# Kernel optimization log

Measured on AMD Instinct MI355X. Metric: run time of the kernel, lower is better.

Reference implementation:

```python
import jax, jax.numpy as jnp
import numpy as np
import math

B, N, E, D = 8, 2048, 2048, 128
MAX_K = 8
HYPER_DIM = 128
LN_EPS = 1e-5


def _sinusoidal_pe(max_pos, dim):
    pe = np.zeros((max_pos, dim), dtype=np.float32)
    position = np.arange(max_pos, dtype=np.float32)[:, None]
    div_term = np.exp(np.arange(0, dim, 2, dtype=np.float32) * (-math.log(10000.0) / dim))
    pe[:, 0::2] = np.sin(position * div_term)
    pe[:, 1::2] = np.cos(position * div_term)
    return jnp.asarray(pe)


def setup_inputs() -> dict:
    key = jax.random.key(0)
    ks = jax.random.split(key, 24)
    s = 0.05
    inp = {
        'x_v': jax.random.normal(ks[0], (B, N, D), jnp.float32),
        'x_e': jax.random.normal(ks[1], (B, E, D), jnp.float32),
        'incidence': (jax.random.uniform(ks[2], (B, N, E), jnp.float32) < 0.01).astype(jnp.float32),
        'suffix_normalizer': jax.random.uniform(ks[3], (B, N), jnp.float32) * 20.0,
        'edge_orders': 1 + jax.random.randint(ks[4], (B, E), 0, MAX_K),
        'node_mask': jax.random.randint(ks[5], (B, N), 0, 2) > 0,
        'edge_mask': jax.random.randint(ks[6], (B, E), 0, 2) > 0,
        'pe1_table': _sinusoidal_pe(MAX_K + 1, D),
        'pe2_table': _sinusoidal_pe(2, D),
        'bias_b': jax.random.uniform(ks[7], (1, D), jnp.float32, -1, 1) / math.sqrt(D),
    }
    i = 8
    for m in ('mlp1', 'mlp2', 'mlp3'):
        inp[m + '_W1'] = jax.random.normal(ks[i], (D, HYPER_DIM), jnp.float32) * s; i += 1
        inp[m + '_b1'] = jnp.zeros((HYPER_DIM,), jnp.float32)
        inp[m + '_W2'] = jax.random.normal(ks[i], (HYPER_DIM, D), jnp.float32) * s; i += 1
        inp[m + '_b2'] = jnp.zeros((D,), jnp.float32)
    for n in ('norm1', 'norm2', 'norm3'):
        inp[n + '_g'] = jnp.ones((D,), jnp.float32)
        inp[n + '_b'] = jnp.zeros((D,), jnp.float32)
    return inp


def _ln(x, g, b):
    mu = jnp.mean(x, axis=-1, keepdims=True)
    var = jnp.mean(jnp.square(x - mu), axis=-1, keepdims=True)
    return (x - mu) * jax.lax.rsqrt(var + LN_EPS) * g + b


def _mlp(x, W1, b1, W2, b2):
    return jax.nn.relu(x @ W1 + b1) @ W2 + b2


def reference(x_v, x_e, incidence, suffix_normalizer, edge_orders, node_mask, edge_mask,
              pe1_table, pe2_table, bias_b,
              mlp1_W1, mlp1_b1, mlp1_W2, mlp1_b2,
              mlp2_W1, mlp2_b1, mlp2_W2, mlp2_b2,
              mlp3_W1, mlp3_b1, mlp3_W2, mlp3_b2,
              norm1_g, norm1_b, norm2_g, norm2_b, norm3_g, norm3_b):
    nm = node_mask[..., None]  # [B,N,1]
    em = edge_mask[..., None]  # [B,E,1]
    x_v = jnp.where(nm, x_v, 0.0)
    x_e = jnp.where(em, x_e, 0.0)
    pe1_k1 = pe1_table[1][None, None, :]          # [1,1,D]
    pe1_k = pe1_table[edge_orders]                # [B,E,D]
    x_v = x_v + _mlp(_ln(x_v, norm1_g, norm1_b) + pe1_k1, mlp1_W1, mlp1_b1, mlp1_W2, mlp1_b2)
    x_e = x_e + _mlp(_ln(x_e, norm1_g, norm1_b) + pe1_k, mlp1_W1, mlp1_b1, mlp1_W2, mlp1_b2)
    x_v = jnp.where(nm, x_v, 0.0)
    x_e = jnp.where(em, x_e, 0.0)
    agg = jnp.einsum('bne,bed->bnd', incidence, x_e)
    x1 = x_v + agg / (1.0 + suffix_normalizer[..., None])
    pe2_s1 = pe2_table[1][None, None, :]
    x1 = x1 + _mlp(_ln(x1, norm2_g, norm2_b) + pe2_s1, mlp2_W1, mlp2_b1, mlp2_W2, mlp2_b2)
    x = jnp.where(nm, x1, 0.0)
    x = x + _mlp(_ln(x, norm3_g, norm3_b), mlp3_W1, mlp3_b1, mlp3_W2, mlp3_b2)
    x = x + bias_b
    x = jnp.where(nm, x, 0.0)
    return x
```

## Files before the change

### kernel.cpp

```cpp
#include <hip/hip_runtime.h>
#include <stdint.h>

#define BB 8
#define NN 2048
#define EE 2048
#define DD 128
#define RBP 132
#define NTHREADS 256
#define WMAT_U32 8192
#define SCANB 4096
#define MLPB 1024
#define LCAP 64

typedef __attribute__((ext_vector_type(8))) short bf16x8;
typedef __attribute__((ext_vector_type(4))) float f32x4;

__device__ inline unsigned bf16rne(float f) {
    unsigned u = __float_as_uint(f);
    return (u + 0x7fffu + ((u >> 16) & 1u)) >> 16;
}
__device__ inline float bf16lo(unsigned u) { return __uint_as_float(u << 16); }
__device__ inline float bf16hi(unsigned u) { return __uint_as_float(u & 0xffff0000u); }

#define SWZ(b) ((b) ^ ((((b) >> 8) & 7) << 4))

struct __align__(16) SmemK1 {
    float rowbuf[32][RBP];
    unsigned h[32 * DD / 2];
    int rmask[32];
    int ords[32];
};

struct __align__(16) SmemK2 {
    float rowbuf[16][RBP];
    unsigned h[16 * DD / 2];
    int rmask[16];
};

__device__ inline void load_rows32(SmemK1& s, const float* __restrict__ src) {
    int t = threadIdx.x;
    for (int idx = t; idx < 32 * 32; idx += NTHREADS) {
        int r = idx >> 5, c4 = (idx & 31) * 4;
        float4 v = *(const float4*)&src[r * DD + c4];
        *(float4*)&s.rowbuf[r][c4] = v;
    }
    __syncthreads();
    for (int idx = t; idx < 32 * 32; idx += NTHREADS) {
        int r = idx >> 5, c4 = (idx & 31) * 4;
        if (s.rmask[r] == 0) *(float4*)&s.rowbuf[r][c4] = make_float4(0.f, 0.f, 0.f, 0.f);
    }
    __syncthreads();
}

__device__ inline void ln32(SmemK1& s, const float* __restrict__ gw,
                            const float* __restrict__ bw,
                            const float* __restrict__ pe_base, bool per_row_pe) {
    int t = threadIdx.x;
    int gr = t >> 3, g = t & 7;
    int base = g * 16;
    float x[16];
    float4* xp = (float4*)x;
    xp[0] = *(const float4*)&s.rowbuf[gr][base + 0];
    xp[1] = *(const float4*)&s.rowbuf[gr][base + 4];
    xp[2] = *(const float4*)&s.rowbuf[gr][base + 8];
    xp[3] = *(const float4*)&s.rowbuf[gr][base + 12];
    float s1 = 0.f, s2 = 0.f;
    #pragma unroll
    for (int i = 0; i < 16; i++) { s1 += x[i]; s2 += x[i] * x[i]; }
    #pragma unroll
    for (int off = 1; off < 8; off <<= 1) {
        s1 += __shfl_xor(s1, off, 64);
        s2 += __shfl_xor(s2, off, 64);
    }
    float mu = s1 * (1.f / 128.f);
    float var = s2 * (1.f / 128.f) - mu * mu;
    float rstd = rsqrtf(var + 1e-5f);
    const float* pe = nullptr;
    if (pe_base) pe = per_row_pe ? (pe_base + (size_t)s.ords[gr] * DD) : pe_base;
    unsigned p[8];
    #pragma unroll
    for (int j = 0; j < 8; j++) {
        int k0 = base + 2 * j;
        float v0 = (x[2 * j] - mu) * rstd * gw[k0] + bw[k0];
        float v1 = (x[2 * j + 1] - mu) * rstd * gw[k0 + 1] + bw[k0 + 1];
        if (pe) { v0 += pe[k0]; v1 += pe[k0 + 1]; }
        p[j] = bf16rne(v0) | (bf16rne(v1) << 16);
    }
    char* hb = (char*)s.h;
    int byte0 = gr * 256 + g * 32;
    uint4 lo = make_uint4(p[0], p[1], p[2], p[3]);
    uint4 hi = make_uint4(p[4], p[5], p[6], p[7]);
    *(uint4*)(hb + SWZ(byte0)) = lo;
    *(uint4*)(hb + SWZ(byte0 + 16)) = hi;
    __syncthreads();
}

template <bool TO_H>
__device__ inline void mm32_f32w(SmemK1& s, const float* __restrict__ Wf,
                                 const float* __restrict__ bias) {
    int t = threadIdx.x;
    int w = t >> 6, l = t & 63;
    int lm = l & 15, lk = l >> 4;
    bf16x8 bfr[2][4];
    #pragma unroll
    for (int nbl = 0; nbl < 2; nbl++) {
        int n = w * 32 + nbl * 16 + lm;
        #pragma unroll
        for (int kb = 0; kb < 4; kb++) {
            int k0 = kb * 32 + lk * 8;
            unsigned pk[4];
            #pragma unroll
            for (int jp = 0; jp < 4; jp++) {
                float a = Wf[(size_t)(k0 + 2 * jp) * DD + n];
                float b = Wf[(size_t)(k0 + 2 * jp + 1) * DD + n];
                pk[jp] = bf16rne(a) | (bf16rne(b) << 16);
            }
            uint4 u = make_uint4(pk[0], pk[1], pk[2], pk[3]);
            bfr[nbl][kb] = *(bf16x8*)&u;
        }
    }
    const char* hb = (const char*)s.h;
    bf16x8 afr[2][4];
    #pragma unroll
    for (int mb = 0; mb < 2; mb++) {
        int row = mb * 16 + lm;
        #pragma unroll
        for (int kb = 0; kb < 4; kb++)
            afr[mb][kb] = *(const bf16x8*)(hb + SWZ(row * 256 + kb * 64 + lk * 16));
    }
    f32x4 acc[2][2];
    #pragma unroll
    for (int mb = 0; mb < 2; mb++)
        #pragma unroll
        for (int nbl = 0; nbl < 2; nbl++)
            acc[mb][nbl] = (f32x4){0.f, 0.f, 0.f, 0.f};
    #pragma unroll
    for (int kb = 0; kb < 4; kb++)
        #pragma unroll
        for (int mb = 0; mb < 2; mb++)
            #pragma unroll
            for (int nbl = 0; nbl < 2; nbl++)
                acc[mb][nbl] = __builtin_amdgcn_mfma_f32_16x16x32_bf16(
                    afr[mb][kb], bfr[nbl][kb], acc[mb][nbl], 0, 0, 0);
    float bcol0 = bias[w * 32 + lm];
    float bcol1 = bias[w * 32 + 16 + lm];
    __syncthreads();
    if (TO_H) {
        char* hw = (char*)s.h;
        #pragma unroll
        for (int mb = 0; mb < 2; mb++)
            #pragma unroll
            for (int nbl = 0; nbl < 2; nbl++) {
                int col = w * 32 + nbl * 16 + lm;
                float bc = nbl ? bcol1 : bcol0;
                #pragma unroll
                for (int j = 0; j < 4; j++) {
                    int row = mb * 16 + lk * 4 + j;
                    float v = fmaxf(acc[mb][nbl][j] + bc, 0.f);
                    *(unsigned short*)(hw + SWZ(row * 256 + col * 2)) =
                        (unsigned short)bf16rne(v);
                }
            }
    } else {
        #pragma unroll
        for (int mb = 0; mb < 2; mb++)
            #pragma unroll
            for (int nbl = 0; nbl < 2; nbl++) {
                int col = w * 32 + nbl * 16 + lm;
                float bc = nbl ? bcol1 : bcol0;
                #pragma unroll
                for (int j = 0; j < 4; j++) {
                    int row = mb * 16 + lk * 4 + j;
                    s.rowbuf[row][col] += acc[mb][nbl][j] + bc;
                }
            }
    }
    __syncthreads();
}

__device__ inline void scan1(const float* __restrict__ inc,
                             const int* __restrict__ nmask,
                             unsigned* __restrict__ lists, int* __restrict__ cnts,
                             int grow) {
    int l = threadIdx.x & 63;
    if (nmask[grow] == 0) return;
    unsigned long long lmlt = (1ull << l) - 1ull;
    const float4* ir = (const float4*)(inc + (size_t)grow * EE);
    float4 v[8];
    #pragma unroll
    for (int i = 0; i < 8; i++) v[i] = ir[l + 64 * i];
    unsigned* lp = lists + (size_t)grow * LCAP;
    int total = 0;
    #pragma unroll
    for (int i = 0; i < 8; i++) {
        #pragma unroll
        for (int c = 0; c < 4; c++) {
            float a = (c == 0) ? v[i].x : (c == 1) ? v[i].y : (c == 2) ? v[i].z : v[i].w;
            bool nz = (a != 0.f);
            unsigned long long msk = __ballot(nz);
            if (nz) {
                int p = total + __popcll(msk & lmlt);
                if (p < LCAP) lp[p] = (unsigned)((l + 64 * i) * 4 + c);
            }
            total += __popcll(msk);
        }
    }
    if (l == 0) cnts[grow] = total > LCAP ? LCAP : total;
}

__device__ inline void ln16(SmemK2& s, const float* __restrict__ gw,
                            const float* __restrict__ bw,
                            const float* __restrict__ pe) {
    int t = threadIdx.x;
    int gr = t >> 4, g = t & 15;
    int base = g * 8;
    float x[8];
    float4* xp = (float4*)x;
    xp[0] = *(const float4*)&s.rowbuf[gr][base + 0];
    xp[1] = *(const float4*)&s.rowbuf[gr][base + 4];
    float s1 = 0.f, s2 = 0.f;
    #pragma unroll
    for (int i = 0; i < 8; i++) { s1 += x[i]; s2 += x[i] * x[i]; }
    #pragma unroll
    for (int off = 1; off < 16; off <<= 1) {
        s1 += __shfl_xor(s1, off, 64);
        s2 += __shfl_xor(s2, off, 64);
    }
    float mu = s1 * (1.f / 128.f);
    float var = s2 * (1.f / 128.f) - mu * mu;
    float rstd = rsqrtf(var + 1e-5f);
    unsigned p[4];
    #pragma unroll
    for (int j = 0; j < 4; j++) {
        int k0 = base + 2 * j;
        float v0 = (x[2 * j] - mu) * rstd * gw[k0] + bw[k0];
        float v1 = (x[2 * j + 1] - mu) * rstd * gw[k0 + 1] + bw[k0 + 1];
        if (pe) { v0 += pe[k0]; v1 += pe[k0 + 1]; }
        p[j] = bf16rne(v0) | (bf16rne(v1) << 16);
    }
    char* hb = (char*)s.h;
    uint4 q = make_uint4(p[0], p[1], p[2], p[3]);
    *(uint4*)(hb + SWZ(gr * 256 + g * 16)) = q;
    __syncthreads();
}

template <bool TO_H>
__device__ inline void mm16(SmemK2& s, const unsigned* __restrict__ WT,
                            const float* __restrict__ bias) {
    int t = threadIdx.x;
    int w = t >> 6, l = t & 63;
    int lm = l & 15, lk = l >> 4;
    bf16x8 bfr[2][4];
    const uint4* wt4 = (const uint4*)WT;
    #pragma unroll
    for (int nbl = 0; nbl < 2; nbl++) {
        int n = w * 32 + nbl * 16 + lm;
        #pragma unroll
        for (int kb = 0; kb < 4; kb++) {
            uint4 u = wt4[n * 16 + kb * 4 + lk];
            bfr[nbl][kb] = *(bf16x8*)&u;
        }
    }
    const char* hb = (const char*)s.h;
    bf16x8 afr[4];
    #pragma unroll
    for (int kb = 0; kb < 4; kb++)
        afr[kb] = *(const bf16x8*)(hb + SWZ(lm * 256 + kb * 64 + lk * 16));
    f32x4 acc[2];
    acc[0] = (f32x4){0.f, 0.f, 0.f, 0.f};
    acc[1] = (f32x4){0.f, 0.f, 0.f, 0.f};
    #pragma unroll
    for (int kb = 0; kb < 4; kb++)
        #pragma unroll
        for (int nbl = 0; nbl < 2; nbl++)
            acc[nbl] = __builtin_amdgcn_mfma_f32_16x16x32_bf16(
                afr[kb], bfr[nbl][kb], acc[nbl], 0, 0, 0);
    float bcol0 = bias[w * 32 + lm];
    float bcol1 = bias[w * 32 + 16 + lm];
    __syncthreads();
    if (TO_H) {
        char* hw = (char*)s.h;
        #pragma unroll
        for (int nbl = 0; nbl < 2; nbl++) {
            int col = w * 32 + nbl * 16 + lm;
            float bc = nbl ? bcol1 : bcol0;
            #pragma unroll
            for (int j = 0; j < 4; j++) {
                int row = lk * 4 + j;
                float v = fmaxf(acc[nbl][j] + bc, 0.f);
                *(unsigned short*)(hw + SWZ(row * 256 + col * 2)) =
                    (unsigned short)bf16rne(v);
            }
        }
    } else {
        #pragma unroll
        for (int nbl = 0; nbl < 2; nbl++) {
            int col = w * 32 + nbl * 16 + lm;
            float bc = nbl ? bcol1 : bcol0;
            #pragma unroll
            for (int j = 0; j < 4; j++) {
                int row = lk * 4 + j;
                s.rowbuf[row][col] += acc[nbl][j] + bc;
            }
        }
    }
    __syncthreads();
}

__device__ inline void gather16(SmemK2& s, int row0,
                                const unsigned* __restrict__ lists,
                                const int* __restrict__ cnts,
                                const unsigned* __restrict__ e2b,
                                const float* __restrict__ sn) {
    int t = threadIdx.x;
    int w = t >> 6, l = t & 63;
    int cnt[4]; unsigned pk[4]; float snv[4];
    #pragma unroll
    for (int i = 0; i < 4; i++) {
        int grow = row0 + w * 4 + i;
        pk[i] = lists[(size_t)grow * LCAP + l];
        snv[i] = sn[grow];
        cnt[i] = cnts[grow];
    }
    #pragma unroll
    for (int i = 0; i < 4; i++) {
        int r = w * 4 + i;
        if (s.rmask[r] == 0) continue;
        int cn = cnt[i]; if (cn > LCAP) cn = LCAP;
        float ax = 0.f, ay = 0.f;
        for (int j0 = 0; j0 < cn; j0 += 8) {
            int nn = cn - j0;
            unsigned uv[8];
            #pragma unroll
            for (int u = 0; u < 8; u++) {
                unsigned e = __shfl(pk[i], j0 + u, 64);
                uv[u] = (u < nn) ? e2b[(size_t)e * 64 + l] : 0u;
            }
            #pragma unroll
            for (int u = 0; u < 8; u++) { ax += bf16lo(uv[u]); ay += bf16hi(uv[u]); }
        }
        float inv = 1.f / (1.f + snv[i]);
        float2* rb = (float2*)&s.rowbuf[r][2 * l];
        float2 cur = *rb;
        cur.x += ax * inv;
        cur.y += ay * inv;
        *rb = cur;
    }
    __syncthreads();
}

__global__ __launch_bounds__(NTHREADS) void k1_kernel(
    const float* __restrict__ x_e, const float* __restrict__ x_v,
    const int* __restrict__ emask, const int* __restrict__ nmask,
    const int* __restrict__ eord, const float* __restrict__ pe1,
    const float* __restrict__ inc,
    const float* __restrict__ n1g, const float* __restrict__ n1b,
    const float* __restrict__ W11, const float* __restrict__ b11,
    const float* __restrict__ W12, const float* __restrict__ b12,
    const float* __restrict__ W21, const float* __restrict__ W22,
    const float* __restrict__ W31, const float* __restrict__ W32,
    unsigned* __restrict__ WT, unsigned* __restrict__ e2pk,
    float* __restrict__ v2out,
    unsigned* __restrict__ lists, int* __restrict__ cnts) {
    int bid = blockIdx.x;
    int t = threadIdx.x;
    if (bid < SCANB) {
        scan1(inc, nmask, lists, cnts, bid * 4 + (t >> 6));
        return;
    }
    __shared__ SmemK1 s;
    int lb = bid - SCANB;
    int gtid = lb * NTHREADS + t;
    if (gtid < 6 * WMAT_U32) {
        int mat = gtid >> 13;
        int idx = gtid & (WMAT_U32 - 1);
        int n = idx >> 6, j = idx & 63;
        const float* W = mat == 0 ? W11 : mat == 1 ? W12 : mat == 2 ? W21
                       : mat == 3 ? W22 : mat == 4 ? W31 : W32;
        float a = W[(2 * j) * DD + n];
        float b = W[(2 * j + 1) * DD + n];
        WT[gtid] = bf16rne(a) | (bf16rne(b) << 16);
    }
    bool isEdge = lb < (BB * EE / 32);
    int mb = isEdge ? lb : lb - (BB * EE / 32);
    int bb = mb & 7;
    int r0 = (mb >> 3) * 32;
    int rowbase = bb * EE + r0;
    const int* mask = isEdge ? emask : nmask;
    if (t < 32) {
        s.rmask[t] = mask[rowbase + t];
        if (isEdge) {
            int o = eord[rowbase + t];
            s.ords[t] = o < 0 ? 0 : (o > 8 ? 8 : o);
        }
    }
    __syncthreads();
    load_rows32(s, (isEdge ? x_e : x_v) + (size_t)rowbase * DD);
    ln32(s, n1g, n1b, isEdge ? pe1 : (pe1 + DD), isEdge);
    mm32_f32w<true>(s, W11, b11);
    mm32_f32w<false>(s, W12, b12);
    if (isEdge) {
        unsigned* dst = e2pk + (size_t)rowbase * (DD / 2);
        for (int idx = t; idx < 32 * 16; idx += NTHREADS) {
            int r = idx >> 4, q = idx & 15;
            uint4 o = make_uint4(0u, 0u, 0u, 0u);
            if (s.rmask[r] != 0) {
                const float* rp = &s.rowbuf[r][q * 8];
                o.x = bf16rne(rp[0]) | (bf16rne(rp[1]) << 16);
                o.y = bf16rne(rp[2]) | (bf16rne(rp[3]) << 16);
                o.z = bf16rne(rp[4]) | (bf16rne(rp[5]) << 16);
                o.w = bf16rne(rp[6]) | (bf16rne(rp[7]) << 16);
            }
            *(uint4*)&dst[r * 64 + q * 4] = o;
        }
    } else {
        for (int idx = t; idx < 32 * 32; idx += NTHREADS) {
            int r = idx >> 5, c4 = (idx & 31) * 4;
            float4 v = make_float4(0.f, 0.f, 0.f, 0.f);
            if (s.rmask[r] != 0) v = *(const float4*)&s.rowbuf[r][c4];
            *(float4*)&v2out[(size_t)(rowbase + r) * DD + c4] = v;
        }
    }
}

__global__ __launch_bounds__(NTHREADS) void k2_kernel(
    const float* __restrict__ v2, const int* __restrict__ nmask,
    const float* __restrict__ sn,
    const float* __restrict__ pe2, const float* __restrict__ biasb,
    const float* __restrict__ n2g, const float* __restrict__ n2b,
    const float* __restrict__ n3g, const float* __restrict__ n3b,
    const unsigned* __restrict__ WT,
    const float* __restrict__ b21, const float* __restrict__ b22,
    const float* __restrict__ b31, const float* __restrict__ b32,
    const unsigned* __restrict__ e2pk, const unsigned* __restrict__ lists,
    const int* __restrict__ cnts, float* __restrict__ out) {
    __shared__ SmemK2 s;
    int bid = blockIdx.x;
    int bb = bid & 7;
    int n0 = (bid >> 3) * 16;
    int row0 = bb * NN + n0;
    int t = threadIdx.x;
    if (t < 16) s.rmask[t] = nmask[row0 + t];
    for (int idx = t; idx < 16 * 32; idx += NTHREADS) {
        int r = idx >> 5, c4 = (idx & 31) * 4;
        float4 v = *(const float4*)&v2[(size_t)(row0 + r) * DD + c4];
        *(float4*)&s.rowbuf[r][c4] = v;
    }
    __syncthreads();
    gather16(s, row0, lists, cnts, e2pk + (size_t)bb * (EE * (DD / 2)), sn);
    ln16(s, n2g, n2b, pe2 + DD);
    mm16<true>(s, WT + 2 * WMAT_U32, b21);
    mm16<false>(s, WT + 3 * WMAT_U32, b22);
    ln16(s, n3g, n3b, nullptr);
    mm16<true>(s, WT + 4 * WMAT_U32, b31);
    mm16<false>(s, WT + 5 * WMAT_U32, b32);
    for (int idx = t; idx < 16 * 32; idx += NTHREADS) {
        int r = idx >> 5, c4 = (idx & 31) * 4;
        float4 v = make_float4(0.f, 0.f, 0.f, 0.f);
        if (s.rmask[r] != 0) {
            v = *(const float4*)&s.rowbuf[r][c4];
            float4 bbv = *(const float4*)&biasb[c4];
            v.x += bbv.x; v.y += bbv.y; v.z += bbv.z; v.w += bbv.w;
        }
        *(float4*)&out[(size_t)(row0 + r) * DD + c4] = v;
    }
}

extern "C" void kernel_launch(void* const* d_in, const int* in_sizes, int n_in,
                              void* d_out, int out_size, void* d_ws, size_t ws_size,
                              hipStream_t stream) {
    const float* x_v   = (const float*)d_in[0];
    const float* x_e   = (const float*)d_in[1];
    const float* inc   = (const float*)d_in[2];
    const float* sn    = (const float*)d_in[3];
    const int*   eord  = (const int*)d_in[4];
    const int*   nmask = (const int*)d_in[5];
    const int*   emask = (const int*)d_in[6];
    const float* pe1   = (const float*)d_in[7];
    const float* pe2   = (const float*)d_in[8];
    const float* biasb = (const float*)d_in[9];
    const float* W11   = (const float*)d_in[10];
    const float* b11   = (const float*)d_in[11];
    const float* W12   = (const float*)d_in[12];
    const float* b12   = (const float*)d_in[13];
    const float* W21   = (const float*)d_in[14];
    const float* b21   = (const float*)d_in[15];
    const float* W22   = (const float*)d_in[16];
    const float* b22   = (const float*)d_in[17];
    const float* W31   = (const float*)d_in[18];
    const float* b31   = (const float*)d_in[19];
    const float* W32   = (const float*)d_in[20];
    const float* b32   = (const float*)d_in[21];
    const float* n1g   = (const float*)d_in[22];
    const float* n1b   = (const float*)d_in[23];
    const float* n2g   = (const float*)d_in[24];
    const float* n2b   = (const float*)d_in[25];
    const float* n3g   = (const float*)d_in[26];
    const float* n3b   = (const float*)d_in[27];

    unsigned* e2pk  = (unsigned*)d_ws;
    unsigned* WT    = e2pk + (size_t)BB * EE * (DD / 2);
    unsigned* lists = WT + 6 * WMAT_U32;
    int*      cnts  = (int*)(lists + (size_t)BB * NN * LCAP);
    float*    out   = (float*)d_out;

    dim3 blk(NTHREADS);
    k1_kernel<<<dim3(SCANB + MLPB), blk, 0, stream>>>(
        x_e, x_v, emask, nmask, eord, pe1, inc,
        n1g, n1b, W11, b11, W12, b12, W21, W22, W31, W32,
        WT, e2pk, out, lists, cnts);
    k2_kernel<<<dim3(BB * NN / 16), blk, 0, stream>>>(
        out, nmask, sn, pe2, biasb,
        n2g, n2b, n3g, n3b,
        WT, b21, b22, b31, b32,
        e2pk, lists, cnts, out);
}
```

Before: 62.92 us.

## Halve rows per block in both kernels and move weight packing to scan blocks

The MLP part of the first kernel now handles 16 rows per block instead of 32, and the second kernel handles 8 rows per block instead of 16, doubling the grid sizes to raise parallelism and shrink per-block shared memory. Packing the four stage-2/3 weight matrices to bf16 moves from the MLP blocks to the scan blocks, and stage-1 weights are no longer pre-packed. In the 8-row kernel the 16x16 MFMA tiles compute half-wasted rows, and every block still reloads and converts weights, so redundant work per output row grows.

```diff
diff --git a/kernel.cpp b/kernel.cpp
--- a/kernel.cpp
+++ b/kernel.cpp
@@ -9,7 +9,6 @@
 #define NTHREADS 256
 #define WMAT_U32 8192
 #define SCANB 4096
-#define MLPB 1024
 #define LCAP 64
 
 typedef __attribute__((ext_vector_type(8))) short bf16x8;
@@ -24,51 +23,34 @@
 
 #define SWZ(b) ((b) ^ ((((b) >> 8) & 7) << 4))
 
-struct __align__(16) SmemK1 {
-    float rowbuf[32][RBP];
-    unsigned h[32 * DD / 2];
-    int rmask[32];
-    int ords[32];
+struct __align__(16) SmemM {
+    float rowbuf[16][RBP];
+    unsigned h[16 * 64];
+    int rmask[16];
+    int ords[16];
 };
 
-struct __align__(16) SmemK2 {
-    float rowbuf[16][RBP];
-    unsigned h[16 * DD / 2];
-    int rmask[16];
+struct __align__(16) SmemG {
+    float rowbuf[8][RBP];
+    unsigned h[16 * 64];
+    int rmask[8];
 };
 
-__device__ inline void load_rows32(SmemK1& s, const float* __restrict__ src) {
-    int t = threadIdx.x;
-    for (int idx = t; idx < 32 * 32; idx += NTHREADS) {
-        int r = idx >> 5, c4 = (idx & 31) * 4;
-        float4 v = *(const float4*)&src[r * DD + c4];
-        *(float4*)&s.rowbuf[r][c4] = v;
-    }
-    __syncthreads();
-    for (int idx = t; idx < 32 * 32; idx += NTHREADS) {
-        int r = idx >> 5, c4 = (idx & 31) * 4;
-        if (s.rmask[r] == 0) *(float4*)&s.rowbuf[r][c4] = make_float4(0.f, 0.f, 0.f, 0.f);
-    }
-    __syncthreads();
-}
-
-__device__ inline void ln32(SmemK1& s, const float* __restrict__ gw,
-                            const float* __restrict__ bw,
+__device__ inline void ln16(float (*rowbuf)[RBP], unsigned* h, const int* ords,
+                            const float* __restrict__ gw, const float* __restrict__ bw,
                             const float* __restrict__ pe_base, bool per_row_pe) {
     int t = threadIdx.x;
-    int gr = t >> 3, g = t & 7;
-    int base = g * 16;
-    float x[16];
+    int gr = t >> 4, g = t & 15;
+    int base = g * 8;
+    float x[8];
     float4* xp = (float4*)x;
-    xp[0] = *(const float4*)&s.rowbuf[gr][base + 0];
-    xp[1] = *(const float4*)&s.rowbuf[gr][base + 4];
-    xp[2] = *(const float4*)&s.rowbuf[gr][base + 8];
-    xp[3] = *(const float4*)&s.rowbuf[gr][base + 12];
+    xp[0] = *(const float4*)&rowbuf[gr][base + 0];
+    xp[1] = *(const float4*)&rowbuf[gr][base + 4];
     float s1 = 0.f, s2 = 0.f;
     #pragma unroll
-    for (int i = 0; i < 16; i++) { s1 += x[i]; s2 += x[i] * x[i]; }
-    #pragma unroll
-    for (int off = 1; off < 8; off <<= 1) {
+    for (int i = 0; i < 8; i++) { s1 += x[i]; s2 += x[i] * x[i]; }
+    #pragma unroll
+    for (int off = 1; off < 16; off <<= 1) {
         s1 += __shfl_xor(s1, off, 64);
         s2 += __shfl_xor(s2, off, 64);
     }
@@ -76,27 +58,24 @@
     float var = s2 * (1.f / 128.f) - mu * mu;
     float rstd = rsqrtf(var + 1e-5f);
     const float* pe = nullptr;
-    if (pe_base) pe = per_row_pe ? (pe_base + (size_t)s.ords[gr] * DD) : pe_base;
-    unsigned p[8];
-    #pragma unroll
-    for (int j = 0; j < 8; j++) {
+    if (pe_base) pe = per_row_pe ? (pe_base + (size_t)ords[gr] * DD) : pe_base;
+    unsigned p[4];
+    #pragma unroll
+    for (int j = 0; j < 4; j++) {
         int k0 = base + 2 * j;
         float v0 = (x[2 * j] - mu) * rstd * gw[k0] + bw[k0];
         float v1 = (x[2 * j + 1] - mu) * rstd * gw[k0 + 1] + bw[k0 + 1];
         if (pe) { v0 += pe[k0]; v1 += pe[k0 + 1]; }
         p[j] = bf16rne(v0) | (bf16rne(v1) << 16);
     }
-    char* hb = (char*)s.h;
-    int byte0 = gr * 256 + g * 32;
-    uint4 lo = make_uint4(p[0], p[1], p[2], p[3]);
-    uint4 hi = make_uint4(p[4], p[5], p[6], p[7]);
-    *(uint4*)(hb + SWZ(byte0)) = lo;
-    *(uint4*)(hb + SWZ(byte0 + 16)) = hi;
+    char* hb = (char*)h;
+    uint4 q = make_uint4(p[0], p[1], p[2], p[3]);
+    *(uint4*)(hb + SWZ(gr * 256 + g * 16)) = q;
     __syncthreads();
 }
 
 template <bool TO_H>
-__device__ inline void mm32_f32w(SmemK1& s, const float* __restrict__ Wf,
+__device__ inline void mm16_f32w(SmemM& s, const float* __restrict__ Wf,
                                  const float* __restrict__ bias) {
     int t = threadIdx.x;
     int w = t >> 6, l = t & 63;
@@ -120,60 +99,186 @@
         }
     }
     const char* hb = (const char*)s.h;
-    bf16x8 afr[2][4];
-    #pragma unroll
-    for (int mb = 0; mb < 2; mb++) {
-        int row = mb * 16 + lm;
-        #pragma unroll
-        for (int kb = 0; kb < 4; kb++)
-            afr[mb][kb] = *(const bf16x8*)(hb + SWZ(row * 256 + kb * 64 + lk * 16));
-    }
-    f32x4 acc[2][2];
-    #pragma unroll
-    for (int mb = 0; mb < 2; mb++)
+    bf16x8 afr[4];
+    #pragma unroll
+    for (int kb = 0; kb < 4; kb++)
+        afr[kb] = *(const bf16x8*)(hb + SWZ(lm * 256 + kb * 64 + lk * 16));
+    f32x4 acc[2];
+    acc[0] = (f32x4){0.f, 0.f, 0.f, 0.f};
+    acc[1] = (f32x4){0.f, 0.f, 0.f, 0.f};
+    #pragma unroll
+    for (int kb = 0; kb < 4; kb++)
         #pragma unroll
         for (int nbl = 0; nbl < 2; nbl++)
-            acc[mb][nbl] = (f32x4){0.f, 0.f, 0.f, 0.f};
-    #pragma unroll
-    for (int kb = 0; kb < 4; kb++)
-        #pragma unroll
-        for (int mb = 0; mb < 2; mb++)
-            #pragma unroll
-            for (int nbl = 0; nbl < 2; nbl++)
-                acc[mb][nbl] = __builtin_amdgcn_mfma_f32_16x16x32_bf16(
-                    afr[mb][kb], bfr[nbl][kb], acc[mb][nbl], 0, 0, 0);
+            acc[nbl] = __builtin_amdgcn_mfma_f32_16x16x32_bf16(
+                afr[kb], bfr[nbl][kb], acc[nbl], 0, 0, 0);
     float bcol0 = bias[w * 32 + lm];
     float bcol1 = bias[w * 32 + 16 + lm];
     __syncthreads();
     if (TO_H) {
         char* hw = (char*)s.h;
         #pragma unroll
-        for (int mb = 0; mb < 2; mb++)
-            #pragma unroll
-            for (int nbl = 0; nbl < 2; nbl++) {
-                int col = w * 32 + nbl * 16 + lm;
-                float bc = nbl ? bcol1 : bcol0;
-                #pragma unroll
-                for (int j = 0; j < 4; j++) {
-                    int row = mb * 16 + lk * 4 + j;
-                    float v = fmaxf(acc[mb][nbl][j] + bc, 0.f);
+        for (int nbl = 0; nbl < 2; nbl++) {
+            int col = w * 32 + nbl * 16 + lm;
+            float bc = nbl ? bcol1 : bcol0;
+            #pragma unroll
+            for (int j = 0; j < 4; j++) {
+                int row = lk * 4 + j;
+                float v = fmaxf(acc[nbl][j] + bc, 0.f);
+                *(unsigned short*)(hw + SWZ(row * 256 + col * 2)) =
+                    (unsigned short)bf16rne(v);
+            }
+        }
+    } else {
+        #pragma unroll
+        for (int nbl = 0; nbl < 2; nbl++) {
+            int col = w * 32 + nbl * 16 + lm;
+            float bc = nbl ? bcol1 : bcol0;
+            #pragma unroll
+            for (int j = 0; j < 4; j++) {
+                int row = lk * 4 + j;
+                s.rowbuf[row][col] += acc[nbl][j] + bc;
+            }
+        }
+    }
+    __syncthreads();
+}
+
+template <bool TO_H>
+__device__ inline void mm8(SmemG& s, const unsigned* __restrict__ WT,
+                           const float* __restrict__ bias) {
+    int t = threadIdx.x;
+    int w = t >> 6, l = t & 63;
+    int lm = l & 15, lk = l >> 4;
+    bf16x8 bfr[2][4];
+    const uint4* wt4 = (const uint4*)WT;
+    #pragma unroll
+    for (int nbl = 0; nbl < 2; nbl++) {
+        int n = w * 32 + nbl * 16 + lm;
+        #pragma unroll
+        for (int kb = 0; kb < 4; kb++) {
+            uint4 u = wt4[n * 16 + kb * 4 + lk];
+            bfr[nbl][kb] = *(bf16x8*)&u;
+        }
+    }
+    const char* hb = (const char*)s.h;
+    bf16x8 afr[4];
+    #pragma unroll
+    for (int kb = 0; kb < 4; kb++)
+        afr[kb] = *(const bf16x8*)(hb + SWZ(lm * 256 + kb * 64 + lk * 16));
+    f32x4 acc[2];
+    acc[0] = (f32x4){0.f, 0.f, 0.f, 0.f};
+    acc[1] = (f32x4){0.f, 0.f, 0.f, 0.f};
+    #pragma unroll
+    for (int kb = 0; kb < 4; kb++)
+        #pragma unroll
+        for (int nbl = 0; nbl < 2; nbl++)
+            acc[nbl] = __builtin_amdgcn_mfma_f32_16x16x32_bf16(
+                afr[kb], bfr[nbl][kb], acc[nbl], 0, 0, 0);
+    float bcol0 = bias[w * 32 + lm];
+    float bcol1 = bias[w * 32 + 16 + lm];
+    __syncthreads();
+    if (TO_H) {
+        char* hw = (char*)s.h;
+        #pragma unroll
+        for (int nbl = 0; nbl < 2; nbl++) {
+            int col = w * 32 + nbl * 16 + lm;
+            float bc = nbl ? bcol1 : bcol0;
+            #pragma unroll
+            for (int j = 0; j < 4; j++) {
+                int row = lk * 4 + j;
+                if (row < 8) {
+                    float v = fmaxf(acc[nbl][j] + bc, 0.f);
                     *(unsigned short*)(hw + SWZ(row * 256 + col * 2)) =
                         (unsigned short)bf16rne(v);
                 }
             }
+        }
     } else {
         #pragma unroll
-        for (int mb = 0; mb < 2; mb++)
-            #pragma unroll
-            for (int nbl = 0; nbl < 2; nbl++) {
-                int col = w * 32 + nbl * 16 + lm;
-                float bc = nbl ? bcol1 : bcol0;
-                #pragma unroll
-                for (int j = 0; j < 4; j++) {
-                    int row = mb * 16 + lk * 4 + j;
-                    s.rowbuf[row][col] += acc[mb][nbl][j] + bc;
-                }
-            }
+        for (int nbl = 0; nbl < 2; nbl++) {
+            int col = w * 32 + nbl * 16 + lm;
+            float bc = nbl ? bcol1 : bcol0;
+            #pragma unroll
+            for (int j = 0; j < 4; j++) {
+                int row = lk * 4 + j;
+                if (row < 8) s.rowbuf[row][col] += acc[nbl][j] + bc;
+            }
+        }
+    }
+    __syncthreads();
+}
+
+__device__ inline void ln8(SmemG& s, const float* __restrict__ gw,
+                           const float* __restrict__ bw,
+                           const float* __restrict__ pe) {
+    int t = threadIdx.x;
+    int gr = t >> 5, g = t & 31;
+    int base = g * 4;
+    float4 xv = *(const float4*)&s.rowbuf[gr][base];
+    float x[4] = {xv.x, xv.y, xv.z, xv.w};
+    float s1 = x[0] + x[1] + x[2] + x[3];
+    float s2 = x[0] * x[0] + x[1] * x[1] + x[2] * x[2] + x[3] * x[3];
+    #pragma unroll
+    for (int off = 1; off < 32; off <<= 1) {
+        s1 += __shfl_xor(s1, off, 64);
+        s2 += __shfl_xor(s2, off, 64);
+    }
+    float mu = s1 * (1.f / 128.f);
+    float var = s2 * (1.f / 128.f) - mu * mu;
+    float rstd = rsqrtf(var + 1e-5f);
+    unsigned p[2];
+    #pragma unroll
+    for (int j = 0; j < 2; j++) {
+        int k0 = base + 2 * j;
+        float v0 = (x[2 * j] - mu) * rstd * gw[k0] + bw[k0];
+        float v1 = (x[2 * j + 1] - mu) * rstd * gw[k0 + 1] + bw[k0 + 1];
+        if (pe) { v0 += pe[k0]; v1 += pe[k0 + 1]; }
+        p[j] = bf16rne(v0) | (bf16rne(v1) << 16);
+    }
+    char* hb = (char*)s.h;
+    *(uint2*)(hb + SWZ(gr * 256 + g * 8)) = make_uint2(p[0], p[1]);
+    __syncthreads();
+}
+
+__device__ inline void gather8(SmemG& s, int row0,
+                               const unsigned* __restrict__ lists,
+                               const int* __restrict__ cnts,
+                               const unsigned* __restrict__ e2b,
+                               const float* __restrict__ sn) {
+    int t = threadIdx.x;
+    int w = t >> 6, l = t & 63;
+    int cnt[2]; unsigned pk[2]; float snv[2];
+    #pragma unroll
+    for (int i = 0; i < 2; i++) {
+        int grow = row0 + w * 2 + i;
+        pk[i] = lists[(size_t)grow * LCAP + l];
+        snv[i] = sn[grow];
+        cnt[i] = cnts[grow];
+    }
+    #pragma unroll
+    for (int i = 0; i < 2; i++) {
+        int r = w * 2 + i;
+        if (s.rmask[r] == 0) continue;
+        int cn = cnt[i]; if (cn > LCAP) cn = LCAP;
+        float ax = 0.f, ay = 0.f;
+        for (int j0 = 0; j0 < cn; j0 += 8) {
+            int nn = cn - j0;
+            unsigned uv[8];
+            #pragma unroll
+            for (int u = 0; u < 8; u++) {
+                unsigned e = __shfl(pk[i], j0 + u, 64);
+                uv[u] = (u < nn) ? e2b[(size_t)e * 64 + l] : 0u;
+            }
+            #pragma unroll
+            for (int u = 0; u < 8; u++) { ax += bf16lo(uv[u]); ay += bf16hi(uv[u]); }
+        }
+        float inv = 1.f / (1.f + snv[i]);
+        float2* rb = (float2*)&s.rowbuf[r][2 * l];
+        float2 cur = *rb;
+        cur.x += ax * inv;
+        cur.y += ay * inv;
+        *rb = cur;
     }
     __syncthreads();
 }
@@ -206,147 +311,6 @@
         }
     }
     if (l == 0) cnts[grow] = total > LCAP ? LCAP : total;
-}
-
-__device__ inline void ln16(SmemK2& s, const float* __restrict__ gw,
-                            const float* __restrict__ bw,
-                            const float* __restrict__ pe) {
-    int t = threadIdx.x;
-    int gr = t >> 4, g = t & 15;
-    int base = g * 8;
-    float x[8];
-    float4* xp = (float4*)x;
-    xp[0] = *(const float4*)&s.rowbuf[gr][base + 0];
-    xp[1] = *(const float4*)&s.rowbuf[gr][base + 4];
-    float s1 = 0.f, s2 = 0.f;
-    #pragma unroll
-    for (int i = 0; i < 8; i++) { s1 += x[i]; s2 += x[i] * x[i]; }
-    #pragma unroll
-    for (int off = 1; off < 16; off <<= 1) {
-        s1 += __shfl_xor(s1, off, 64);
-        s2 += __shfl_xor(s2, off, 64);
-    }
-    float mu = s1 * (1.f / 128.f);
-    float var = s2 * (1.f / 128.f) - mu * mu;
-    float rstd = rsqrtf(var + 1e-5f);
-    unsigned p[4];
-    #pragma unroll
-    for (int j = 0; j < 4; j++) {
-        int k0 = base + 2 * j;
-        float v0 = (x[2 * j] - mu) * rstd * gw[k0] + bw[k0];
-        float v1 = (x[2 * j + 1] - mu) * rstd * gw[k0 + 1] + bw[k0 + 1];
-        if (pe) { v0 += pe[k0]; v1 += pe[k0 + 1]; }
-        p[j] = bf16rne(v0) | (bf16rne(v1) << 16);
-    }
-    char* hb = (char*)s.h;
-    uint4 q = make_uint4(p[0], p[1], p[2], p[3]);
-    *(uint4*)(hb + SWZ(gr * 256 + g * 16)) = q;
-    __syncthreads();
-}
-
-template <bool TO_H>
-__device__ inline void mm16(SmemK2& s, const unsigned* __restrict__ WT,
-                            const float* __restrict__ bias) {
-    int t = threadIdx.x;
-    int w = t >> 6, l = t & 63;
-    int lm = l & 15, lk = l >> 4;
-    bf16x8 bfr[2][4];
-    const uint4* wt4 = (const uint4*)WT;
-    #pragma unroll
-    for (int nbl = 0; nbl < 2; nbl++) {
-        int n = w * 32 + nbl * 16 + lm;
-        #pragma unroll
-        for (int kb = 0; kb < 4; kb++) {
-            uint4 u = wt4[n * 16 + kb * 4 + lk];
-            bfr[nbl][kb] = *(bf16x8*)&u;
-        }
-    }
-    const char* hb = (const char*)s.h;
-    bf16x8 afr[4];
-    #pragma unroll
-    for (int kb = 0; kb < 4; kb++)
-        afr[kb] = *(const bf16x8*)(hb + SWZ(lm * 256 + kb * 64 + lk * 16));
-    f32x4 acc[2];
-    acc[0] = (f32x4){0.f, 0.f, 0.f, 0.f};
-    acc[1] = (f32x4){0.f, 0.f, 0.f, 0.f};
-    #pragma unroll
-    for (int kb = 0; kb < 4; kb++)
-        #pragma unroll
-        for (int nbl = 0; nbl < 2; nbl++)
-            acc[nbl] = __builtin_amdgcn_mfma_f32_16x16x32_bf16(
-                afr[kb], bfr[nbl][kb], acc[nbl], 0, 0, 0);
-    float bcol0 = bias[w * 32 + lm];
-    float bcol1 = bias[w * 32 + 16 + lm];
-    __syncthreads();
-    if (TO_H) {
-        char* hw = (char*)s.h;
-        #pragma unroll
-        for (int nbl = 0; nbl < 2; nbl++) {
-            int col = w * 32 + nbl * 16 + lm;
-            float bc = nbl ? bcol1 : bcol0;
-            #pragma unroll
-            for (int j = 0; j < 4; j++) {
-                int row = lk * 4 + j;
-                float v = fmaxf(acc[nbl][j] + bc, 0.f);
-                *(unsigned short*)(hw + SWZ(row * 256 + col * 2)) =
-                    (unsigned short)bf16rne(v);
-            }
-        }
-    } else {
-        #pragma unroll
-        for (int nbl = 0; nbl < 2; nbl++) {
-            int col = w * 32 + nbl * 16 + lm;
-            float bc = nbl ? bcol1 : bcol0;
-            #pragma unroll
-            for (int j = 0; j < 4; j++) {
-                int row = lk * 4 + j;
-                s.rowbuf[row][col] += acc[nbl][j] + bc;
-            }
-        }
-    }
-    __syncthreads();
-}
-
-__device__ inline void gather16(SmemK2& s, int row0,
-                                const unsigned* __restrict__ lists,
-                                const int* __restrict__ cnts,
-                                const unsigned* __restrict__ e2b,
-                                const float* __restrict__ sn) {
-    int t = threadIdx.x;
-    int w = t >> 6, l = t & 63;
-    int cnt[4]; unsigned pk[4]; float snv[4];
-    #pragma unroll
-    for (int i = 0; i < 4; i++) {
-        int grow = row0 + w * 4 + i;
-        pk[i] = lists[(size_t)grow * LCAP + l];
-        snv[i] = sn[grow];
-        cnt[i] = cnts[grow];
-    }
-    #pragma unroll
-    for (int i = 0; i < 4; i++) {
-        int r = w * 4 + i;
-        if (s.rmask[r] == 0) continue;
-        int cn = cnt[i]; if (cn > LCAP) cn = LCAP;
-        float ax = 0.f, ay = 0.f;
-        for (int j0 = 0; j0 < cn; j0 += 8) {
-            int nn = cn - j0;
-            unsigned uv[8];
-            #pragma unroll
-            for (int u = 0; u < 8; u++) {
-                unsigned e = __shfl(pk[i], j0 + u, 64);
-                uv[u] = (u < nn) ? e2b[(size_t)e * 64 + l] : 0u;
-            }
-            #pragma unroll
-            for (int u = 0; u < 8; u++) { ax += bf16lo(uv[u]); ay += bf16hi(uv[u]); }
-        }
-        float inv = 1.f / (1.f + snv[i]);
-        float2* rb = (float2*)&s.rowbuf[r][2 * l];
-        float2 cur = *rb;
-        cur.x += ax * inv;
-        cur.y += ay * inv;
-        *rb = cur;
-    }
-    __syncthreads();
 }
 
 __global__ __launch_bounds__(NTHREADS) void k1_kernel(
@@ -365,29 +329,28 @@
     int bid = blockIdx.x;
     int t = threadIdx.x;
     if (bid < SCANB) {
+        int gtid = bid * NTHREADS + t;
+        if (gtid < 4 * WMAT_U32) {
+            int mat = gtid >> 13;
+            int idx = gtid & (WMAT_U32 - 1);
+            int n = idx >> 6, j = idx & 63;
+            const float* W = mat == 0 ? W21 : mat == 1 ? W22 : mat == 2 ? W31 : W32;
+            float a = W[(2 * j) * DD + n];
+            float b = W[(2 * j + 1) * DD + n];
+            WT[gtid] = bf16rne(a) | (bf16rne(b) << 16);
+        }
         scan1(inc, nmask, lists, cnts, bid * 4 + (t >> 6));
         return;
     }
-    __shared__ SmemK1 s;
+    __shared__ SmemM s;
     int lb = bid - SCANB;
-    int gtid = lb * NTHREADS + t;
-    if (gtid < 6 * WMAT_U32) {
-        int mat = gtid >> 13;
-        int idx = gtid & (WMAT_U32 - 1);
-        int n = idx >> 6, j = idx & 63;
-        const float* W = mat == 0 ? W11 : mat == 1 ? W12 : mat == 2 ? W21
-                       : mat == 3 ? W22 : mat == 4 ? W31 : W32;
-        float a = W[(2 * j) * DD + n];
-        float b = W[(2 * j + 1) * DD + n];
-        WT[gtid] = bf16rne(a) | (bf16rne(b) << 16);
-    }
-    bool isEdge = lb < (BB * EE / 32);
-    int mb = isEdge ? lb : lb - (BB * EE / 32);
+    bool isEdge = lb < (BB * EE / 16);
+    int mb = isEdge ? lb : lb - (BB * EE / 16);
     int bb = mb & 7;
-    int r0 = (mb >> 3) * 32;
+    int r0 = (mb >> 3) * 16;
     int rowbase = bb * EE + r0;
     const int* mask = isEdge ? emask : nmask;
-    if (t < 32) {
+    if (t < 16) {
         s.rmask[t] = mask[rowbase + t];
         if (isEdge) {
             int o = eord[rowbase + t];
@@ -395,13 +358,23 @@
         }
     }
     __syncthreads();
-    load_rows32(s, (isEdge ? x_e : x_v) + (size_t)rowbase * DD);
-    ln32(s, n1g, n1b, isEdge ? pe1 : (pe1 + DD), isEdge);
-    mm32_f32w<true>(s, W11, b11);
-    mm32_f32w<false>(s, W12, b12);
+    for (int idx = t; idx < 16 * 32; idx += NTHREADS) {
+        int r = idx >> 5, c4 = (idx & 31) * 4;
+        float4 v = *(const float4*)&((isEdge ? x_e : x_v))[(size_t)(rowbase + r) * DD + c4];
+        *(float4*)&s.rowbuf[r][c4] = v;
+    }
+    __syncthreads();
+    for (int idx = t; idx < 16 * 32; idx += NTHREADS) {
+        int r = idx >> 5, c4 = (idx & 31) * 4;
+        if (s.rmask[r] == 0) *(float4*)&s.rowbuf[r][c4] = make_float4(0.f, 0.f, 0.f, 0.f);
+    }
+    __syncthreads();
+    ln16(s.rowbuf, s.h, s.ords, n1g, n1b, isEdge ? pe1 : (pe1 + DD), isEdge);
+    mm16_f32w<true>(s, W11, b11);
+    mm16_f32w<false>(s, W12, b12);
     if (isEdge) {
         unsigned* dst = e2pk + (size_t)rowbase * (DD / 2);
-        for (int idx = t; idx < 32 * 16; idx += NTHREADS) {
+        for (int idx = t; idx < 16 * 16; idx += NTHREADS) {
             int r = idx >> 4, q = idx & 15;
             uint4 o = make_uint4(0u, 0u, 0u, 0u);
             if (s.rmask[r] != 0) {
@@ -414,7 +387,7 @@
             *(uint4*)&dst[r * 64 + q * 4] = o;
         }
     } else {
-        for (int idx = t; idx < 32 * 32; idx += NTHREADS) {
+        for (int idx = t; idx < 16 * 32; idx += NTHREADS) {
             int r = idx >> 5, c4 = (idx & 31) * 4;
             float4 v = make_float4(0.f, 0.f, 0.f, 0.f);
             if (s.rmask[r] != 0) v = *(const float4*)&s.rowbuf[r][c4];
@@ -434,28 +407,28 @@
     const float* __restrict__ b31, const float* __restrict__ b32,
     const unsigned* __restrict__ e2pk, const unsigned* __restrict__ lists,
     const int* __restrict__ cnts, float* __restrict__ out) {
-    __shared__ SmemK2 s;
+    __shared__ SmemG s;
     int bid = blockIdx.x;
     int bb = bid & 7;
-    int n0 = (bid >> 3) * 16;
+    int n0 = (bid >> 3) * 8;
     int row0 = bb * NN + n0;
     int t = threadIdx.x;
-    if (t < 16) s.rmask[t] = nmask[row0 + t];
-    for (int idx = t; idx < 16 * 32; idx += NTHREADS) {
-        int r = idx >> 5, c4 = (idx & 31) * 4;
+    if (t < 8) s.rmask[t] = nmask[row0 + t];
+    {
+        int r = t >> 5, c4 = (t & 31) * 4;
         float4 v = *(const float4*)&v2[(size_t)(row0 + r) * DD + c4];
         *(float4*)&s.rowbuf[r][c4] = v;
     }
     __syncthreads();
-    gather16(s, row0, lists, cnts, e2pk + (size_t)bb * (EE * (DD / 2)), sn);
-    ln16(s, n2g, n2b, pe2 + DD);
-    mm16<true>(s, WT + 2 * WMAT_U32, b21);
-    mm16<false>(s, WT + 3 * WMAT_U32, b22);
-    ln16(s, n3g, n3b, nullptr);
-    mm16<true>(s, WT + 4 * WMAT_U32, b31);
-    mm16<false>(s, WT + 5 * WMAT_U32, b32);
-    for (int idx = t; idx < 16 * 32; idx += NTHREADS) {
-        int r = idx >> 5, c4 = (idx & 31) * 4;
+    gather8(s, row0, lists, cnts, e2pk + (size_t)bb * (EE * (DD / 2)), sn);
+    ln8(s, n2g, n2b, pe2 + DD);
+    mm8<true>(s, WT + 0 * WMAT_U32, b21);
+    mm8<false>(s, WT + 1 * WMAT_U32, b22);
+    ln8(s, n3g, n3b, nullptr);
+    mm8<true>(s, WT + 2 * WMAT_U32, b31);
+    mm8<false>(s, WT + 3 * WMAT_U32, b32);
+    {
+        int r = t >> 5, c4 = (t & 31) * 4;
         float4 v = make_float4(0.f, 0.f, 0.f, 0.f);
         if (s.rmask[r] != 0) {
             v = *(const float4*)&s.rowbuf[r][c4];
@@ -500,16 +473,16 @@
 
     unsigned* e2pk  = (unsigned*)d_ws;
     unsigned* WT    = e2pk + (size_t)BB * EE * (DD / 2);
-    unsigned* lists = WT + 6 * WMAT_U32;
+    unsigned* lists = WT + 4 * WMAT_U32;
     int*      cnts  = (int*)(lists + (size_t)BB * NN * LCAP);
     float*    out   = (float*)d_out;
 
     dim3 blk(NTHREADS);
-    k1_kernel<<<dim3(SCANB + MLPB), blk, 0, stream>>>(
+    k1_kernel<<<dim3(SCANB + 2 * BB * EE / 16), blk, 0, stream>>>(
         x_e, x_v, emask, nmask, eord, pe1, inc,
         n1g, n1b, W11, b11, W12, b12, W21, W22, W31, W32,
         WT, e2pk, out, lists, cnts);
-    k2_kernel<<<dim3(BB * NN / 16), blk, 0, stream>>>(
+    k2_kernel<<<dim3(BB * NN / 8), blk, 0, stream>>>(
         out, nmask, sn, pe2, biasb,
         n2g, n2b, n3g, n3b,
         WT, b21, b22, b31, b32,
```

New measurement: 84.33 us. +34.0%, slower.

## Fuse incidence scan with edge gather into a per-row kernel, split node MLPs

Applied to the files above, without the earlier changes.

Moves the incidence-row scan out of the first kernel into a new middle kernel. There, each wave scans one node row, keeps the nonzero edge list in LDS and immediately gathers and sums the packed edge features. The result goes to an fp32 aggregation buffer that the final MLP kernel adds in. This drops the global lists/counts round trip and lets the gather latency overlap with the scan. In exchange the scan no longer overlaps the edge/node MLP work, it adds a third launch, and it writes and reads an extra aggregation buffer.

```diff
diff --git a/kernel.cpp b/kernel.cpp
--- a/kernel.cpp
+++ b/kernel.cpp
@@ -8,8 +8,6 @@
 #define RBP 132
 #define NTHREADS 256
 #define WMAT_U32 8192
-#define SCANB 4096
-#define MLPB 1024
 #define LCAP 64
 
 typedef __attribute__((ext_vector_type(8))) short bf16x8;
@@ -26,14 +24,14 @@
 
 struct __align__(16) SmemK1 {
     float rowbuf[32][RBP];
-    unsigned h[32 * DD / 2];
+    unsigned h[32 * 64];
     int rmask[32];
     int ords[32];
 };
 
-struct __align__(16) SmemK2 {
+struct __align__(16) SmemK3 {
     float rowbuf[16][RBP];
-    unsigned h[16 * DD / 2];
+    unsigned h[16 * 64];
     int rmask[16];
 };
 
@@ -178,37 +176,7 @@
     __syncthreads();
 }
 
-__device__ inline void scan1(const float* __restrict__ inc,
-                             const int* __restrict__ nmask,
-                             unsigned* __restrict__ lists, int* __restrict__ cnts,
-                             int grow) {
-    int l = threadIdx.x & 63;
-    if (nmask[grow] == 0) return;
-    unsigned long long lmlt = (1ull << l) - 1ull;
-    const float4* ir = (const float4*)(inc + (size_t)grow * EE);
-    float4 v[8];
-    #pragma unroll
-    for (int i = 0; i < 8; i++) v[i] = ir[l + 64 * i];
-    unsigned* lp = lists + (size_t)grow * LCAP;
-    int total = 0;
-    #pragma unroll
-    for (int i = 0; i < 8; i++) {
-        #pragma unroll
-        for (int c = 0; c < 4; c++) {
-            float a = (c == 0) ? v[i].x : (c == 1) ? v[i].y : (c == 2) ? v[i].z : v[i].w;
-            bool nz = (a != 0.f);
-            unsigned long long msk = __ballot(nz);
-            if (nz) {
-                int p = total + __popcll(msk & lmlt);
-                if (p < LCAP) lp[p] = (unsigned)((l + 64 * i) * 4 + c);
-            }
-            total += __popcll(msk);
-        }
-    }
-    if (l == 0) cnts[grow] = total > LCAP ? LCAP : total;
-}
-
-__device__ inline void ln16(SmemK2& s, const float* __restrict__ gw,
+__device__ inline void ln16(SmemK3& s, const float* __restrict__ gw,
                             const float* __restrict__ bw,
                             const float* __restrict__ pe) {
     int t = threadIdx.x;
@@ -245,7 +213,7 @@
 }
 
 template <bool TO_H>
-__device__ inline void mm16(SmemK2& s, const unsigned* __restrict__ WT,
+__device__ inline void mm16(SmemK3& s, const unsigned* __restrict__ WT,
                             const float* __restrict__ bias) {
     int t = threadIdx.x;
     int w = t >> 6, l = t & 63;
@@ -307,82 +275,32 @@
     __syncthreads();
 }
 
-__device__ inline void gather16(SmemK2& s, int row0,
-                                const unsigned* __restrict__ lists,
-                                const int* __restrict__ cnts,
-                                const unsigned* __restrict__ e2b,
-                                const float* __restrict__ sn) {
-    int t = threadIdx.x;
-    int w = t >> 6, l = t & 63;
-    int cnt[4]; unsigned pk[4]; float snv[4];
-    #pragma unroll
-    for (int i = 0; i < 4; i++) {
-        int grow = row0 + w * 4 + i;
-        pk[i] = lists[(size_t)grow * LCAP + l];
-        snv[i] = sn[grow];
-        cnt[i] = cnts[grow];
-    }
-    #pragma unroll
-    for (int i = 0; i < 4; i++) {
-        int r = w * 4 + i;
-        if (s.rmask[r] == 0) continue;
-        int cn = cnt[i]; if (cn > LCAP) cn = LCAP;
-        float ax = 0.f, ay = 0.f;
-        for (int j0 = 0; j0 < cn; j0 += 8) {
-            int nn = cn - j0;
-            unsigned uv[8];
-            #pragma unroll
-            for (int u = 0; u < 8; u++) {
-                unsigned e = __shfl(pk[i], j0 + u, 64);
-                uv[u] = (u < nn) ? e2b[(size_t)e * 64 + l] : 0u;
-            }
-            #pragma unroll
-            for (int u = 0; u < 8; u++) { ax += bf16lo(uv[u]); ay += bf16hi(uv[u]); }
-        }
-        float inv = 1.f / (1.f + snv[i]);
-        float2* rb = (float2*)&s.rowbuf[r][2 * l];
-        float2 cur = *rb;
-        cur.x += ax * inv;
-        cur.y += ay * inv;
-        *rb = cur;
-    }
-    __syncthreads();
-}
-
 __global__ __launch_bounds__(NTHREADS) void k1_kernel(
     const float* __restrict__ x_e, const float* __restrict__ x_v,
     const int* __restrict__ emask, const int* __restrict__ nmask,
     const int* __restrict__ eord, const float* __restrict__ pe1,
-    const float* __restrict__ inc,
     const float* __restrict__ n1g, const float* __restrict__ n1b,
     const float* __restrict__ W11, const float* __restrict__ b11,
     const float* __restrict__ W12, const float* __restrict__ b12,
     const float* __restrict__ W21, const float* __restrict__ W22,
     const float* __restrict__ W31, const float* __restrict__ W32,
     unsigned* __restrict__ WT, unsigned* __restrict__ e2pk,
-    float* __restrict__ v2out,
-    unsigned* __restrict__ lists, int* __restrict__ cnts) {
+    float* __restrict__ v2out) {
+    __shared__ SmemK1 s;
     int bid = blockIdx.x;
     int t = threadIdx.x;
-    if (bid < SCANB) {
-        scan1(inc, nmask, lists, cnts, bid * 4 + (t >> 6));
-        return;
-    }
-    __shared__ SmemK1 s;
-    int lb = bid - SCANB;
-    int gtid = lb * NTHREADS + t;
-    if (gtid < 6 * WMAT_U32) {
+    int gtid = bid * NTHREADS + t;
+    if (gtid < 4 * WMAT_U32) {
         int mat = gtid >> 13;
         int idx = gtid & (WMAT_U32 - 1);
         int n = idx >> 6, j = idx & 63;
-        const float* W = mat == 0 ? W11 : mat == 1 ? W12 : mat == 2 ? W21
-                       : mat == 3 ? W22 : mat == 4 ? W31 : W32;
+        const float* W = mat == 0 ? W21 : mat == 1 ? W22 : mat == 2 ? W31 : W32;
         float a = W[(2 * j) * DD + n];
         float b = W[(2 * j + 1) * DD + n];
         WT[gtid] = bf16rne(a) | (bf16rne(b) << 16);
     }
-    bool isEdge = lb < (BB * EE / 32);
-    int mb = isEdge ? lb : lb - (BB * EE / 32);
+    bool isEdge = bid < (BB * EE / 32);
+    int mb = isEdge ? bid : bid - (BB * EE / 32);
     int bb = mb & 7;
     int r0 = (mb >> 3) * 32;
     int rowbase = bb * EE + r0;
@@ -424,17 +342,66 @@
 }
 
 __global__ __launch_bounds__(NTHREADS) void k2_kernel(
+    const float* __restrict__ inc, const int* __restrict__ nmask,
+    const float* __restrict__ sn, const unsigned* __restrict__ e2pk,
+    float* __restrict__ agg) {
+    __shared__ unsigned scw[4][64];
+    int wib = threadIdx.x >> 6, l = threadIdx.x & 63;
+    int grow = blockIdx.x * 4 + wib;
+    if (grow >= BB * NN) return;
+    if (nmask[grow] == 0) return;
+    unsigned long long lmlt = (1ull << l) - 1ull;
+    const float4* ir = (const float4*)(inc + (size_t)grow * EE);
+    float4 v[8];
+    #pragma unroll
+    for (int i = 0; i < 8; i++) v[i] = ir[l + 64 * i];
+    unsigned* sc = scw[wib];
+    int total = 0;
+    #pragma unroll
+    for (int i = 0; i < 8; i++) {
+        #pragma unroll
+        for (int c = 0; c < 4; c++) {
+            float a = (c == 0) ? v[i].x : (c == 1) ? v[i].y : (c == 2) ? v[i].z : v[i].w;
+            bool nz = (a != 0.f);
+            unsigned long long msk = __ballot(nz);
+            if (nz) {
+                int p = total + __popcll(msk & lmlt);
+                if (p < LCAP) sc[p] = (unsigned)((l + 64 * i) * 4 + c);
+            }
+            total += __popcll(msk);
+        }
+    }
+    if (total > LCAP) total = LCAP;
+    asm volatile("s_waitcnt lgkmcnt(0)" ::: "memory");
+    unsigned pk = (l < total) ? sc[l] : 0u;
+    const unsigned* e2b = e2pk + (size_t)(grow >> 11) * (EE * (DD / 2));
+    float ax = 0.f, ay = 0.f;
+    for (int j0 = 0; j0 < total; j0 += 8) {
+        int nn = total - j0;
+        unsigned uv[8];
+        #pragma unroll
+        for (int u = 0; u < 8; u++) {
+            unsigned e = __shfl(pk, j0 + u, 64);
+            uv[u] = (u < nn) ? e2b[(size_t)e * 64 + l] : 0u;
+        }
+        #pragma unroll
+        for (int u = 0; u < 8; u++) { ax += bf16lo(uv[u]); ay += bf16hi(uv[u]); }
+    }
+    float inv = 1.f / (1.f + sn[grow]);
+    *(float2*)&agg[(size_t)grow * DD + 2 * l] = make_float2(ax * inv, ay * inv);
+}
+
+__global__ __launch_bounds__(NTHREADS) void k3_kernel(
     const float* __restrict__ v2, const int* __restrict__ nmask,
-    const float* __restrict__ sn,
+    const float* __restrict__ agg,
     const float* __restrict__ pe2, const float* __restrict__ biasb,
     const float* __restrict__ n2g, const float* __restrict__ n2b,
     const float* __restrict__ n3g, const float* __restrict__ n3b,
     const unsigned* __restrict__ WT,
     const float* __restrict__ b21, const float* __restrict__ b22,
     const float* __restrict__ b31, const float* __restrict__ b32,
-    const unsigned* __restrict__ e2pk, const unsigned* __restrict__ lists,
-    const int* __restrict__ cnts, float* __restrict__ out) {
-    __shared__ SmemK2 s;
+    float* __restrict__ out) {
+    __shared__ SmemK3 s;
     int bid = blockIdx.x;
     int bb = bid & 7;
     int n0 = (bid >> 3) * 16;
@@ -447,13 +414,23 @@
         *(float4*)&s.rowbuf[r][c4] = v;
     }
     __syncthreads();
-    gather16(s, row0, lists, cnts, e2pk + (size_t)bb * (EE * (DD / 2)), sn);
+    for (int idx = t; idx < 16 * 32; idx += NTHREADS) {
+        int r = idx >> 5, c4 = (idx & 31) * 4;
+        if (s.rmask[r] != 0) {
+            float4 a = *(const float4*)&agg[(size_t)(row0 + r) * DD + c4];
+            float4* rb = (float4*)&s.rowbuf[r][c4];
+            float4 cur = *rb;
+            cur.x += a.x; cur.y += a.y; cur.z += a.z; cur.w += a.w;
+            *rb = cur;
+        }
+    }
+    __syncthreads();
     ln16(s, n2g, n2b, pe2 + DD);
-    mm16<true>(s, WT + 2 * WMAT_U32, b21);
-    mm16<false>(s, WT + 3 * WMAT_U32, b22);
+    mm16<true>(s, WT + 0 * WMAT_U32, b21);
+    mm16<false>(s, WT + 1 * WMAT_U32, b22);
     ln16(s, n3g, n3b, nullptr);
-    mm16<true>(s, WT + 4 * WMAT_U32, b31);
-    mm16<false>(s, WT + 5 * WMAT_U32, b32);
+    mm16<true>(s, WT + 2 * WMAT_U32, b31);
+    mm16<false>(s, WT + 3 * WMAT_U32, b32);
     for (int idx = t; idx < 16 * 32; idx += NTHREADS) {
         int r = idx >> 5, c4 = (idx & 31) * 4;
         float4 v = make_float4(0.f, 0.f, 0.f, 0.f);
@@ -498,20 +475,20 @@
     const float* n3g   = (const float*)d_in[26];
     const float* n3b   = (const float*)d_in[27];
 
-    unsigned* e2pk  = (unsigned*)d_ws;
-    unsigned* WT    = e2pk + (size_t)BB * EE * (DD / 2);
-    unsigned* lists = WT + 6 * WMAT_U32;
-    int*      cnts  = (int*)(lists + (size_t)BB * NN * LCAP);
-    float*    out   = (float*)d_out;
+    unsigned* e2pk = (unsigned*)d_ws;
+    unsigned* WT   = e2pk + (size_t)BB * EE * (DD / 2);
+    float*    agg  = (float*)(WT + 4 * WMAT_U32);
+    float*    out  = (float*)d_out;
 
     dim3 blk(NTHREADS);
-    k1_kernel<<<dim3(SCANB + MLPB), blk, 0, stream>>>(
-        x_e, x_v, emask, nmask, eord, pe1, inc,
+    k1_kernel<<<dim3(2 * BB * EE / 32), blk, 0, stream>>>(
+        x_e, x_v, emask, nmask, eord, pe1,
         n1g, n1b, W11, b11, W12, b12, W21, W22, W31, W32,
-        WT, e2pk, out, lists, cnts);
-    k2_kernel<<<dim3(BB * NN / 16), blk, 0, stream>>>(
-        out, nmask, sn, pe2, biasb,
+        WT, e2pk, out);
+    k2_kernel<<<dim3(BB * NN / 4), blk, 0, stream>>>(
+        inc, nmask, sn, e2pk, agg);
+    k3_kernel<<<dim3(BB * NN / 16), blk, 0, stream>>>(
+        out, nmask, agg, pe2, biasb,
         n2g, n2b, n3g, n3b,
-        WT, b21, b22, b31, b32,
-        e2pk, lists, cnts, out);
-}
+        WT, b21, b22, b31, b32, out);
+}
```

Result: slower. 64.19 us (+2.0%).
